# Performance work log

Measured on AMD Instinct MI355X. Metric: run time of the kernel, lower is better.

The kernel has to match this reference:

```python
import jax, jax.numpy as jnp
import numpy as np


def setup_inputs() -> dict:
    key = jax.random.key(0)
    kx, kw = jax.random.split(key)
    x = jax.random.normal(kx, (4096, 4096), dtype=jnp.float32)
    weight = jax.random.uniform(kw, (7, 7), dtype=jnp.float32)
    bias = jnp.zeros((1,), dtype=jnp.float32)
    return {"x": x, "weight": weight, "bias": bias}


def reference(x, weight, bias):
    # Valid 2D cross-correlation (stride 1, no padding) + scalar bias,
    # identical math to corr2d(X, K) + bias in the torch module.
    lhs = x[None, None, :, :]          # [N=1, C=1, H, W]
    rhs = weight[None, None, :, :]     # [O=1, I=1, kh, kw]
    y = jax.lax.conv_general_dilated(
        lhs, rhs,
        window_strides=(1, 1),
        padding='VALID',
        dimension_numbers=('NCHW', 'OIHW', 'NCHW'),
    )
    return y[0, 0] + bias[0]  # [H-kh+1, W-kw+1]
```

## Files before the change

### kernel.cpp

```cpp
#include <hip/hip_runtime.h>

#define TILE_W 128
#define TILE_H 64
#define HALO   6
#define IN_H   (TILE_H + HALO)
#define LDS_W  136
#define N      4096
#define ON     4090

__device__ __forceinline__ void gload_lds4(const float* g, float* l) {
    __builtin_amdgcn_global_load_lds(
        (const __attribute__((address_space(1))) void*)g,
        (__attribute__((address_space(3))) void*)l,
        4, 0, 0);
}

__global__ __launch_bounds__(256, 4)
void conv7x7_kernel(const float* __restrict__ x,
                    const float* __restrict__ w,
                    const float* __restrict__ bias,
                    float* __restrict__ out)
{
    __shared__ float tile[IN_H][LDS_W];

    const int tid  = threadIdx.x;
    const int lane = tid & 63;
    const int wv   = tid >> 6;
    const int x0   = blockIdx.x * TILE_W;
    const int y0   = blockIdx.y * TILE_H;

    {
        const int gx2 = min(x0 + 128 + lane, N - 1);
        for (int r = wv; r < IN_H; r += 4) {
            const int gy = min(y0 + r, N - 1);
            const float* rowp = x + (size_t)gy * N;
            gload_lds4(rowp + x0 + lane,      &tile[r][0]);
            gload_lds4(rowp + x0 + 64 + lane, &tile[r][64]);
            if (lane < 8)
                gload_lds4(rowp + gx2,        &tile[r][128]);
        }
    }

    float ws[49];
    #pragma unroll
    for (int i = 0; i < 49; ++i) ws[i] = w[i];
    const float bv = bias[0];

    __syncthreads();

    const int tx = (tid & 15) * 8;
    const int ty = (tid >> 4) * 4;

    float acc[4][8] = {};

    #pragma unroll
    for (int rr = 0; rr < 10; ++rr) {
        const float* row = &tile[ty + rr][tx];
        float v[14];
        const float4 a = *reinterpret_cast<const float4*>(row);
        const float4 b = *reinterpret_cast<const float4*>(row + 4);
        const float4 c = *reinterpret_cast<const float4*>(row + 8);
        const float2 d = *reinterpret_cast<const float2*>(row + 12);
        v[0]=a.x;  v[1]=a.y;  v[2]=a.z;  v[3]=a.w;
        v[4]=b.x;  v[5]=b.y;  v[6]=b.z;  v[7]=b.w;
        v[8]=c.x;  v[9]=c.y;  v[10]=c.z; v[11]=c.w;
        v[12]=d.x; v[13]=d.y;

        #pragma unroll
        for (int r = 0; r < 4; ++r) {
            const int ky = rr - r;
            if (ky >= 0 && ky < 7) {
                #pragma unroll
                for (int kx = 0; kx < 7; ++kx) {
                    const float wk = ws[ky * 7 + kx];
                    #pragma unroll
                    for (int j = 0; j < 8; ++j)
                        acc[r][j] = fmaf(v[kx + j], wk, acc[r][j]);
                }
            }
        }
    }

    const int ox0 = x0 + tx;
    const int oy0 = y0 + ty;
    if (ox0 + 8 <= ON && oy0 + 4 <= ON) {
        #pragma unroll
        for (int r = 0; r < 4; ++r) {
            float* dst = out + (size_t)(oy0 + r) * ON + ox0;
            #pragma unroll
            for (int j = 0; j < 4; ++j) {
                const float2 t = make_float2(acc[r][2*j] + bv, acc[r][2*j+1] + bv);
                *reinterpret_cast<float2*>(dst + 2*j) = t;
            }
        }
    } else {
        #pragma unroll
        for (int r = 0; r < 4; ++r) {
            const int oy = oy0 + r;
            if (oy < ON) {
                float* dst = out + (size_t)oy * ON;
                #pragma unroll
                for (int j = 0; j < 8; ++j) {
                    const int ox = ox0 + j;
                    if (ox < ON) dst[ox] = acc[r][j] + bv;
                }
            }
        }
    }
}

extern "C" void kernel_launch(void* const* d_in, const int* in_sizes, int n_in,
                              void* d_out, int out_size, void* d_ws, size_t ws_size,
                              hipStream_t stream) {
    const float* x    = (const float*)d_in[0];
    const float* w    = (const float*)d_in[1];
    const float* bias = (const float*)d_in[2];
    float* out        = (float*)d_out;

    dim3 grid((ON + TILE_W - 1) / TILE_W, (ON + TILE_H - 1) / TILE_H);
    conv7x7_kernel<<<grid, dim3(256, 1, 1), 0, stream>>>(x, w, bias, out);
}
```

Baseline: 41.86 us.

## Use 16-byte global-to-LDS loads and remap thread tiles to 8x4 outputs

```diff
diff --git a/kernel.cpp b/kernel.cpp
--- a/kernel.cpp
+++ b/kernel.cpp
@@ -5,14 +5,18 @@
 #define HALO   6
 #define IN_H   (TILE_H + HALO)
 #define LDS_W  136
-#define N      4096
-#define ON     4090
+#define CPR    (LDS_W / 4)
+#define TILE_CHUNKS (IN_H * CPR)
+#define STAGE_INSTR ((TILE_CHUNKS + 63) / 64)
+#define LDS_FLOATS  (STAGE_INSTR * 64 * 4)
+#define N  4096
+#define ON 4090
 
-__device__ __forceinline__ void gload_lds4(const float* g, float* l) {
+__device__ __forceinline__ void gload_lds16(const float* g, float* l) {
     __builtin_amdgcn_global_load_lds(
         (const __attribute__((address_space(1))) void*)g,
         (__attribute__((address_space(3))) void*)l,
-        4, 0, 0);
+        16, 0, 0);
 }
 
 __global__ __launch_bounds__(256, 4)
@@ -21,7 +25,7 @@
                     const float* __restrict__ bias,
                     float* __restrict__ out)
 {
-    __shared__ float tile[IN_H][LDS_W];
+    __shared__ float tile[LDS_FLOATS];
 
     const int tid  = threadIdx.x;
     const int lane = tid & 63;
@@ -30,14 +34,15 @@
     const int y0   = blockIdx.y * TILE_H;
 
     {
-        const int gx2 = min(x0 + 128 + lane, N - 1);
-        for (int r = wv; r < IN_H; r += 4) {
-            const int gy = min(y0 + r, N - 1);
-            const float* rowp = x + (size_t)gy * N;
-            gload_lds4(rowp + x0 + lane,      &tile[r][0]);
-            gload_lds4(rowp + x0 + 64 + lane, &tile[r][64]);
-            if (lane < 8)
-                gload_lds4(rowp + gx2,        &tile[r][128]);
+        const int xc0 = x0 >> 2;
+        for (int k = wv; k < STAGE_INSTR; k += 4) {
+            const int m   = (k << 6) + lane;
+            const int row = m / CPR;
+            const int cc  = m - row * CPR;
+            const int gy  = min(y0 + row, N - 1);
+            const int gc  = min(xc0 + cc, (N >> 2) - 1);
+            const float* src = x + ((size_t)gy << 12) + ((size_t)gc << 2);
+            gload_lds16(src, tile + (k << 8));
         }
     }
 
@@ -48,61 +53,58 @@
 
     __syncthreads();
 
-    const int tx = (tid & 15) * 8;
-    const int ty = (tid >> 4) * 4;
+    const int tau   = tid & 31;
+    const int rg    = tid >> 5;
+    const int colf  = tau << 2;
+    const int rbase = rg << 3;
 
-    float acc[4][8] = {};
+    float acc[8][4] = {};
 
     #pragma unroll
-    for (int rr = 0; rr < 10; ++rr) {
-        const float* row = &tile[ty + rr][tx];
-        float v[14];
-        const float4 a = *reinterpret_cast<const float4*>(row);
-        const float4 b = *reinterpret_cast<const float4*>(row + 4);
-        const float4 c = *reinterpret_cast<const float4*>(row + 8);
-        const float2 d = *reinterpret_cast<const float2*>(row + 12);
-        v[0]=a.x;  v[1]=a.y;  v[2]=a.z;  v[3]=a.w;
-        v[4]=b.x;  v[5]=b.y;  v[6]=b.z;  v[7]=b.w;
-        v[8]=c.x;  v[9]=c.y;  v[10]=c.z; v[11]=c.w;
-        v[12]=d.x; v[13]=d.y;
+    for (int rr = 0; rr < 14; ++rr) {
+        const float* rp = tile + (rbase + rr) * LDS_W + colf;
+        float v[10];
+        const float4 a = *reinterpret_cast<const float4*>(rp);
+        const float4 b = *reinterpret_cast<const float4*>(rp + 4);
+        const float2 c = *reinterpret_cast<const float2*>(rp + 8);
+        v[0]=a.x; v[1]=a.y; v[2]=a.z; v[3]=a.w;
+        v[4]=b.x; v[5]=b.y; v[6]=b.z; v[7]=b.w;
+        v[8]=c.x; v[9]=c.y;
 
         #pragma unroll
-        for (int r = 0; r < 4; ++r) {
+        for (int r = 0; r < 8; ++r) {
             const int ky = rr - r;
             if (ky >= 0 && ky < 7) {
                 #pragma unroll
                 for (int kx = 0; kx < 7; ++kx) {
                     const float wk = ws[ky * 7 + kx];
                     #pragma unroll
-                    for (int j = 0; j < 8; ++j)
+                    for (int j = 0; j < 4; ++j)
                         acc[r][j] = fmaf(v[kx + j], wk, acc[r][j]);
                 }
             }
         }
     }
 
-    const int ox0 = x0 + tx;
-    const int oy0 = y0 + ty;
-    if (ox0 + 8 <= ON && oy0 + 4 <= ON) {
+    const int ox  = x0 + colf;
+    const int oy0 = y0 + rbase;
+    if (ox + 4 <= ON && oy0 + 8 <= ON) {
         #pragma unroll
-        for (int r = 0; r < 4; ++r) {
-            float* dst = out + (size_t)(oy0 + r) * ON + ox0;
-            #pragma unroll
-            for (int j = 0; j < 4; ++j) {
-                const float2 t = make_float2(acc[r][2*j] + bv, acc[r][2*j+1] + bv);
-                *reinterpret_cast<float2*>(dst + 2*j) = t;
-            }
+        for (int r = 0; r < 8; ++r) {
+            float* dst = out + (size_t)(oy0 + r) * ON + ox;
+            *reinterpret_cast<float2*>(dst)     = make_float2(acc[r][0] + bv, acc[r][1] + bv);
+            *reinterpret_cast<float2*>(dst + 2) = make_float2(acc[r][2] + bv, acc[r][3] + bv);
         }
     } else {
         #pragma unroll
-        for (int r = 0; r < 4; ++r) {
+        for (int r = 0; r < 8; ++r) {
             const int oy = oy0 + r;
             if (oy < ON) {
                 float* dst = out + (size_t)oy * ON;
                 #pragma unroll
-                for (int j = 0; j < 8; ++j) {
-                    const int ox = ox0 + j;
-                    if (ox < ON) dst[ox] = acc[r][j] + bv;
+                for (int j = 0; j < 4; ++j) {
+                    const int oxj = ox + j;
+                    if (oxj < ON) dst[oxj] = acc[r][j] + bv;
                 }
             }
         }
```

New measurement: 37.14 us. 1.13x faster.
